# Kernel tuning notes

Measured on AMD Instinct MI355X. Metric: run time of the kernel, lower is better.

The kernel has to match this reference:

```python
import jax, jax.numpy as jnp
import numpy as np

N = 8192
MARGIN = 0.2
LAMB = 0.012
ITERS = 5


def setup_inputs() -> dict:
    key = jax.random.key(0)
    # sims in [0,1): cosine-similarity-like scores; exp(-(1-s)/lamb) needs s near [0,1]
    sims = jax.random.uniform(key, (N, N), dtype=jnp.float32)
    return {"sims": sims}


def _ot(sims):
    # Sinkhorn-Knopp normalization, r = c = ones so (r/u) == 1/u, (c/v) == 1/v
    P = jnp.exp(-(1.0 - sims) / LAMB)
    P = P / jnp.sum(P)  # global normalization (dims [-2,-1])
    for _ in range(ITERS):
        u = P.sum(axis=-1, keepdims=True)   # row sums  [N,1]
        P = P / u
        v = P.sum(axis=-2, keepdims=True)   # col sums  [1,N]
        P = P / v
    return P


def reference(sims):
    P = _ot(sims)
    d = jnp.diagonal(P)                     # [N]
    eye = jnp.eye(P.shape[0], dtype=bool)
    # cost_im: anchor = column diagonal (d[j]); cost_s: anchor = row diagonal (d[i])
    cost_im = jnp.where(eye, 0.0, jnp.maximum(P - d[None, :] + MARGIN, 0.0))
    cost_s = jnp.where(eye, 0.0, jnp.maximum(P - d[:, None] + MARGIN, 0.0))
    # max_violation = False -> sum over all hinge terms
    return cost_s.sum() + cost_im.sum()
```

## Files before the change

### kernel.cpp

```cpp
#include <hip/hip_runtime.h>


#define NN 8192u
#define MARGIN 0.2f
#define KF (1.4426950408889634f / 0.012f)

__device__ __forceinline__ float blk_reduce(float v, float* red) {
#pragma unroll
  for (int off = 32; off; off >>= 1) v += __shfl_down(v, off, 64);
  const int lane = threadIdx.x & 63, wid = threadIdx.x >> 6;
  __syncthreads();
  if (lane == 0) red[wid] = v;
  __syncthreads();
  return red[0] + red[1] + red[2] + red[3];
}

__device__ __forceinline__ void unpk4(uint q, float& f0, float& f1, float& f2,
                                      float& f3) {
  auto lo = __builtin_amdgcn_cvt_pk_f32_fp8((int)q, false);
  auto hi = __builtin_amdgcn_cvt_pk_f32_fp8((int)q, true);
  f0 = lo[0]; f1 = lo[1]; f2 = hi[0]; f3 = hi[1];
}

template <bool USEQ>
__global__ __launch_bounds__(256) void k_pass0(const float* __restrict__ sims,
                                               uint* __restrict__ Qw,
                                               float* __restrict__ R) {
  __shared__ float red[4];
  const uint row = blockIdx.x;
  const uint t = threadIdx.x;
  float acc = 0.f;
#pragma unroll
  for (uint ch = 0; ch < 8; ++ch) {
    const uint col = ch * 1024u + t * 4u;
    const float4 s = *(const float4*)(sims + row * NN + col);
    const float p0 = exp2f((s.x - 1.f) * KF);
    const float p1 = exp2f((s.y - 1.f) * KF);
    const float p2 = exp2f((s.z - 1.f) * KF);
    const float p3 = exp2f((s.w - 1.f) * KF);
    if constexpr (USEQ) {
      int pk = 0;
      pk = __builtin_amdgcn_cvt_pk_fp8_f32(p0, p1, pk, false);
      pk = __builtin_amdgcn_cvt_pk_fp8_f32(p2, p3, pk, true);
      Qw[(row * NN + col) >> 2] = (uint)pk;
      float q0, q1, q2, q3;
      unpk4((uint)pk, q0, q1, q2, q3);
      acc += (q0 + q1) + (q2 + q3);
    } else {
      acc += (p0 + p1) + (p2 + p3);
    }
  }
  const float s = blk_reduce(acc, red);
  if (t == 0) R[row] = 1.f / s;
}

template <bool USEQ>
__global__ __launch_bounds__(256) void k_colmv(const float* __restrict__ sims,
                                               const uint* __restrict__ Qw,
                                               const float* __restrict__ R,
                                               float* __restrict__ part) {
  const uint t = threadIdx.x;
  const uint col = blockIdx.x * 1024u + t * 4u;
  const uint row0 = blockIdx.y * 128u;
  float a0 = 0.f, a1 = 0.f, a2 = 0.f, a3 = 0.f;
  for (uint rr = 0; rr < 128u; ++rr) {
    const uint row = row0 + rr;
    const float Rr = R[row];
    if constexpr (USEQ) {
      float f0, f1, f2, f3;
      unpk4(Qw[(row * NN + col) >> 2], f0, f1, f2, f3);
      a0 += f0 * Rr; a1 += f1 * Rr; a2 += f2 * Rr; a3 += f3 * Rr;
    } else {
      const float4 s = *(const float4*)(sims + row * NN + col);
      a0 += exp2f((s.x - 1.f) * KF) * Rr;
      a1 += exp2f((s.y - 1.f) * KF) * Rr;
      a2 += exp2f((s.z - 1.f) * KF) * Rr;
      a3 += exp2f((s.w - 1.f) * KF) * Rr;
    }
  }
  float4 o; o.x = a0; o.y = a1; o.z = a2; o.w = a3;
  *(float4*)(part + blockIdx.y * NN + col) = o;
}

template <bool USEQ>
__global__ __launch_bounds__(256) void k_colred(const float* __restrict__ part,
                                                float* __restrict__ Cg, int fin,
                                                const float* __restrict__ sims,
                                                const uint* __restrict__ Qw,
                                                const float* __restrict__ R,
                                                float* __restrict__ dvec,
                                                float* __restrict__ out) {
  const uint j = blockIdx.x * 256u + threadIdx.x;
  float s = 0.f;
#pragma unroll 8
  for (uint r = 0; r < 64u; ++r) s += part[r * NN + j];
  const float c = 1.f / s;
  Cg[j] = c;
  if (fin) {
    float pd;
    if constexpr (USEQ) {
      const uint u = Qw[(j * 8193u) >> 2];
      const uint b = (u >> ((j & 3u) * 8u)) & 0xFFu;
      pd = __builtin_amdgcn_cvt_f32_fp8((int)b, 0);
    } else {
      pd = exp2f((sims[j * 8193u] - 1.f) * KF);
    }
    dvec[j] = pd * R[j] * c;
    if (j == 0) *out = 0.f;
  }
}

template <bool USEQ>
__global__ __launch_bounds__(256) void k_rowmv(const float* __restrict__ sims,
                                               const uint* __restrict__ Qw,
                                               const float* __restrict__ Cg,
                                               float* __restrict__ R) {
  __shared__ float ldsC[NN];
  __shared__ float red[4];
  const uint t = threadIdx.x;
  for (uint c = t * 4u; c < NN; c += 1024u)
    *(float4*)(ldsC + c) = *(const float4*)(Cg + c);
  __syncthreads();
#pragma unroll
  for (uint r = 0; r < 4u; ++r) {
    const uint row = blockIdx.x * 4u + r;
    float acc = 0.f;
#pragma unroll
    for (uint ch = 0; ch < 2u; ++ch) {
      const uint col = ch * 4096u + t * 16u;
      const float4 c0 = *(const float4*)(ldsC + col);
      const float4 c1 = *(const float4*)(ldsC + col + 4);
      const float4 c2 = *(const float4*)(ldsC + col + 8);
      const float4 c3 = *(const float4*)(ldsC + col + 12);
      if constexpr (USEQ) {
        const uint4 q = *(const uint4*)(Qw + row * 2048u + (col >> 2));
        float a0, a1, a2, a3, b0, b1, b2, b3;
        unpk4(q.x, a0, a1, a2, a3);
        unpk4(q.y, b0, b1, b2, b3);
        acc += a0 * c0.x + a1 * c0.y + a2 * c0.z + a3 * c0.w;
        acc += b0 * c1.x + b1 * c1.y + b2 * c1.z + b3 * c1.w;
        unpk4(q.z, a0, a1, a2, a3);
        unpk4(q.w, b0, b1, b2, b3);
        acc += a0 * c2.x + a1 * c2.y + a2 * c2.z + a3 * c2.w;
        acc += b0 * c3.x + b1 * c3.y + b2 * c3.z + b3 * c3.w;
      } else {
        const float* sp = sims + row * NN + col;
        const float4 s0 = *(const float4*)(sp);
        const float4 s1 = *(const float4*)(sp + 4);
        const float4 s2 = *(const float4*)(sp + 8);
        const float4 s3 = *(const float4*)(sp + 12);
        acc += exp2f((s0.x - 1.f) * KF) * c0.x + exp2f((s0.y - 1.f) * KF) * c0.y +
               exp2f((s0.z - 1.f) * KF) * c0.z + exp2f((s0.w - 1.f) * KF) * c0.w;
        acc += exp2f((s1.x - 1.f) * KF) * c1.x + exp2f((s1.y - 1.f) * KF) * c1.y +
               exp2f((s1.z - 1.f) * KF) * c1.z + exp2f((s1.w - 1.f) * KF) * c1.w;
        acc += exp2f((s2.x - 1.f) * KF) * c2.x + exp2f((s2.y - 1.f) * KF) * c2.y +
               exp2f((s2.z - 1.f) * KF) * c2.z + exp2f((s2.w - 1.f) * KF) * c2.w;
        acc += exp2f((s3.x - 1.f) * KF) * c3.x + exp2f((s3.y - 1.f) * KF) * c3.y +
               exp2f((s3.z - 1.f) * KF) * c3.z + exp2f((s3.w - 1.f) * KF) * c3.w;
      }
    }
    const float s = blk_reduce(acc, red);
    if (t == 0) R[row] = 1.f / s;
  }
}

template <bool USEQ>
__global__ __launch_bounds__(256) void k_loss(const float* __restrict__ sims,
                                              const uint* __restrict__ Qw,
                                              const float* __restrict__ R,
                                              const float* __restrict__ Cg,
                                              const float* __restrict__ dvec,
                                              float* __restrict__ out) {
  __shared__ float red[4];
  const uint t = threadIdx.x;
  const uint col = blockIdx.x * 1024u + t * 4u;
  const uint row0 = blockIdx.y * 128u;
  const float4 c4 = *(const float4*)(Cg + col);
  const float4 d4 = *(const float4*)(dvec + col);
  float acc = 0.f;
  for (uint rr = 0; rr < 128u; ++rr) {
    const uint row = row0 + rr;
    const float Rr = R[row];
    const float dr = dvec[row];
    float f0, f1, f2, f3;
    if constexpr (USEQ) {
      unpk4(Qw[(row * NN + col) >> 2], f0, f1, f2, f3);
    } else {
      const float4 s = *(const float4*)(sims + row * NN + col);
      f0 = exp2f((s.x - 1.f) * KF);
      f1 = exp2f((s.y - 1.f) * KF);
      f2 = exp2f((s.z - 1.f) * KF);
      f3 = exp2f((s.w - 1.f) * KF);
    }
    float p, h;
    p = f0 * Rr * c4.x;
    h = fmaxf(p - d4.x + MARGIN, 0.f) + fmaxf(p - dr + MARGIN, 0.f);
    acc += (row == col + 0u) ? 0.f : h;
    p = f1 * Rr * c4.y;
    h = fmaxf(p - d4.y + MARGIN, 0.f) + fmaxf(p - dr + MARGIN, 0.f);
    acc += (row == col + 1u) ? 0.f : h;
    p = f2 * Rr * c4.z;
    h = fmaxf(p - d4.z + MARGIN, 0.f) + fmaxf(p - dr + MARGIN, 0.f);
    acc += (row == col + 2u) ? 0.f : h;
    p = f3 * Rr * c4.w;
    h = fmaxf(p - d4.w + MARGIN, 0.f) + fmaxf(p - dr + MARGIN, 0.f);
    acc += (row == col + 3u) ? 0.f : h;
  }
  const float s = blk_reduce(acc, red);
  if (t == 0) atomicAdd(out, s);
}

template <bool USEQ>
static void run_all(const float* sims, float* out, void* ws, hipStream_t stream) {
  uint* Qw;
  float* R;
  if (USEQ) {
    Qw = (uint*)ws;
    R = (float*)((char*)ws + (size_t)NN * NN);
  } else {
    Qw = nullptr;
    R = (float*)ws;
  }
  float* C = R + NN;
  float* dv = C + NN;
  float* part = dv + NN;

  k_pass0<USEQ><<<8192, 256, 0, stream>>>(sims, Qw, R);
  for (int it = 0; it < 5; ++it) {
    k_colmv<USEQ><<<dim3(8, 64), 256, 0, stream>>>(sims, Qw, R, part);
    k_colred<USEQ><<<32, 256, 0, stream>>>(part, C, (it == 4) ? 1 : 0, sims, Qw,
                                           R, dv, out);
    if (it < 4) k_rowmv<USEQ><<<2048, 256, 0, stream>>>(sims, Qw, C, R);
  }
  k_loss<USEQ><<<dim3(8, 64), 256, 0, stream>>>(sims, Qw, R, C, dv, out);
}

extern "C" void kernel_launch(void* const* d_in, const int* in_sizes, int n_in,
                              void* d_out, int out_size, void* d_ws,
                              size_t ws_size, hipStream_t stream) {
  const float* sims = (const float*)d_in[0];
  float* out = (float*)d_out;
  const size_t need_q =
      (size_t)NN * NN + (size_t)(3 * NN + 64 * NN) * sizeof(float);
  if (ws_size >= need_q) {
    run_all<true>(sims, out, d_ws, stream);
  } else {
    run_all<false>(sims, out, d_ws, stream);
  }
}
```

Before: 538.5 us.

## Retune Sinkhorn kernels: more column-split blocks, vectorized row reduce, nontemporal loads

The column matvec now splits rows into 128 chunks of 64 instead of 64 chunks of 128, giving more blocks and more partial sums. The column-reduce kernel uses 1024 threads and combines the partials in shared memory. The row matvec drops the 8192-float LDS staging of column scales and instead processes four rows at once with coalesced per-row loads and a 4-way shuffle reduction. It also adds a nontemporal load for sims in pass0 and unroll pragmas, which could trade register pressure and workspace size for better occupancy and memory-level parallelism.

Result: faster. 485.7 us (-9.8%).

```diff
diff --git a/kernel.cpp b/kernel.cpp
--- a/kernel.cpp
+++ b/kernel.cpp
@@ -4,6 +4,8 @@
 #define NN 8192u
 #define MARGIN 0.2f
 #define KF (1.4426950408889634f / 0.012f)
+
+typedef float f32x4 __attribute__((ext_vector_type(4)));
 
 __device__ __forceinline__ float blk_reduce(float v, float* red) {
 #pragma unroll
@@ -33,11 +35,12 @@
 #pragma unroll
   for (uint ch = 0; ch < 8; ++ch) {
     const uint col = ch * 1024u + t * 4u;
-    const float4 s = *(const float4*)(sims + row * NN + col);
-    const float p0 = exp2f((s.x - 1.f) * KF);
-    const float p1 = exp2f((s.y - 1.f) * KF);
-    const float p2 = exp2f((s.z - 1.f) * KF);
-    const float p3 = exp2f((s.w - 1.f) * KF);
+    const f32x4 s =
+        __builtin_nontemporal_load((const f32x4*)(sims + row * NN + col));
+    const float p0 = exp2f((s[0] - 1.f) * KF);
+    const float p1 = exp2f((s[1] - 1.f) * KF);
+    const float p2 = exp2f((s[2] - 1.f) * KF);
+    const float p3 = exp2f((s[3] - 1.f) * KF);
     if constexpr (USEQ) {
       int pk = 0;
       pk = __builtin_amdgcn_cvt_pk_fp8_f32(p0, p1, pk, false);
@@ -61,9 +64,10 @@
                                                float* __restrict__ part) {
   const uint t = threadIdx.x;
   const uint col = blockIdx.x * 1024u + t * 4u;
-  const uint row0 = blockIdx.y * 128u;
+  const uint row0 = blockIdx.y * 64u;
   float a0 = 0.f, a1 = 0.f, a2 = 0.f, a3 = 0.f;
-  for (uint rr = 0; rr < 128u; ++rr) {
+#pragma unroll 8
+  for (uint rr = 0; rr < 64u; ++rr) {
     const uint row = row0 + rr;
     const float Rr = R[row];
     if constexpr (USEQ) {
@@ -83,30 +87,40 @@
 }
 
 template <bool USEQ>
-__global__ __launch_bounds__(256) void k_colred(const float* __restrict__ part,
-                                                float* __restrict__ Cg, int fin,
-                                                const float* __restrict__ sims,
-                                                const uint* __restrict__ Qw,
-                                                const float* __restrict__ R,
-                                                float* __restrict__ dvec,
-                                                float* __restrict__ out) {
-  const uint j = blockIdx.x * 256u + threadIdx.x;
+__global__ __launch_bounds__(1024) void k_colred(const float* __restrict__ part,
+                                                 float* __restrict__ Cg, int fin,
+                                                 const float* __restrict__ sims,
+                                                 const uint* __restrict__ Qw,
+                                                 const float* __restrict__ R,
+                                                 float* __restrict__ dvec,
+                                                 float* __restrict__ out) {
+  __shared__ float red2[3][256];
+  const uint t = threadIdx.x;
+  const uint lj = t & 255u;
+  const uint q = t >> 8;
+  const uint j = blockIdx.x * 256u + lj;
   float s = 0.f;
+  const uint r0 = q * 32u;
 #pragma unroll 8
-  for (uint r = 0; r < 64u; ++r) s += part[r * NN + j];
-  const float c = 1.f / s;
-  Cg[j] = c;
-  if (fin) {
-    float pd;
-    if constexpr (USEQ) {
-      const uint u = Qw[(j * 8193u) >> 2];
-      const uint b = (u >> ((j & 3u) * 8u)) & 0xFFu;
-      pd = __builtin_amdgcn_cvt_f32_fp8((int)b, 0);
-    } else {
-      pd = exp2f((sims[j * 8193u] - 1.f) * KF);
-    }
-    dvec[j] = pd * R[j] * c;
-    if (j == 0) *out = 0.f;
+  for (uint r = r0; r < r0 + 32u; ++r) s += part[r * NN + j];
+  if (q) red2[q - 1][lj] = s;
+  __syncthreads();
+  if (q == 0) {
+    s += red2[0][lj] + red2[1][lj] + red2[2][lj];
+    const float c = 1.f / s;
+    Cg[j] = c;
+    if (fin) {
+      float pd;
+      if constexpr (USEQ) {
+        const uint u = Qw[(j * 8193u) >> 2];
+        const uint b = (u >> ((j & 3u) * 8u)) & 0xFFu;
+        pd = __builtin_amdgcn_cvt_f32_fp8((int)b, 0);
+      } else {
+        pd = exp2f((sims[j * 8193u] - 1.f) * KF);
+      }
+      dvec[j] = pd * R[j] * c;
+      if (j == 0) *out = 0.f;
+    }
   }
 }
 
@@ -115,52 +129,55 @@
                                                const uint* __restrict__ Qw,
                                                const float* __restrict__ Cg,
                                                float* __restrict__ R) {
-  __shared__ float ldsC[NN];
-  __shared__ float red[4];
-  const uint t = threadIdx.x;
-  for (uint c = t * 4u; c < NN; c += 1024u)
-    *(float4*)(ldsC + c) = *(const float4*)(Cg + c);
-  __syncthreads();
-#pragma unroll
-  for (uint r = 0; r < 4u; ++r) {
-    const uint row = blockIdx.x * 4u + r;
-    float acc = 0.f;
-#pragma unroll
-    for (uint ch = 0; ch < 2u; ++ch) {
-      const uint col = ch * 4096u + t * 16u;
-      const float4 c0 = *(const float4*)(ldsC + col);
-      const float4 c1 = *(const float4*)(ldsC + col + 4);
-      const float4 c2 = *(const float4*)(ldsC + col + 8);
-      const float4 c3 = *(const float4*)(ldsC + col + 12);
-      if constexpr (USEQ) {
-        const uint4 q = *(const uint4*)(Qw + row * 2048u + (col >> 2));
-        float a0, a1, a2, a3, b0, b1, b2, b3;
-        unpk4(q.x, a0, a1, a2, a3);
-        unpk4(q.y, b0, b1, b2, b3);
-        acc += a0 * c0.x + a1 * c0.y + a2 * c0.z + a3 * c0.w;
-        acc += b0 * c1.x + b1 * c1.y + b2 * c1.z + b3 * c1.w;
-        unpk4(q.z, a0, a1, a2, a3);
-        unpk4(q.w, b0, b1, b2, b3);
-        acc += a0 * c2.x + a1 * c2.y + a2 * c2.z + a3 * c2.w;
-        acc += b0 * c3.x + b1 * c3.y + b2 * c3.z + b3 * c3.w;
-      } else {
-        const float* sp = sims + row * NN + col;
-        const float4 s0 = *(const float4*)(sp);
-        const float4 s1 = *(const float4*)(sp + 4);
-        const float4 s2 = *(const float4*)(sp + 8);
-        const float4 s3 = *(const float4*)(sp + 12);
-        acc += exp2f((s0.x - 1.f) * KF) * c0.x + exp2f((s0.y - 1.f) * KF) * c0.y +
-               exp2f((s0.z - 1.f) * KF) * c0.z + exp2f((s0.w - 1.f) * KF) * c0.w;
-        acc += exp2f((s1.x - 1.f) * KF) * c1.x + exp2f((s1.y - 1.f) * KF) * c1.y +
-               exp2f((s1.z - 1.f) * KF) * c1.z + exp2f((s1.w - 1.f) * KF) * c1.w;
-        acc += exp2f((s2.x - 1.f) * KF) * c2.x + exp2f((s2.y - 1.f) * KF) * c2.y +
-               exp2f((s2.z - 1.f) * KF) * c2.z + exp2f((s2.w - 1.f) * KF) * c2.w;
-        acc += exp2f((s3.x - 1.f) * KF) * c3.x + exp2f((s3.y - 1.f) * KF) * c3.y +
-               exp2f((s3.z - 1.f) * KF) * c3.z + exp2f((s3.w - 1.f) * KF) * c3.w;
-      }
-    }
-    const float s = blk_reduce(acc, red);
-    if (t == 0) R[row] = 1.f / s;
+  __shared__ float red[4][4];
+  const uint t = threadIdx.x;
+  const uint row0 = blockIdx.x * 4u;
+  float a0 = 0.f, a1 = 0.f, a2 = 0.f, a3 = 0.f;
+#pragma unroll
+  for (uint it = 0; it < 8u; ++it) {
+    const uint col = it * 1024u + t * 4u;
+    const float4 c = *(const float4*)(Cg + col);
+    if constexpr (USEQ) {
+      const uint base = (row0 * NN + col) >> 2;
+      float f0, f1, f2, f3;
+      unpk4(Qw[base         ], f0, f1, f2, f3);
+      a0 += f0 * c.x + f1 * c.y + f2 * c.z + f3 * c.w;
+      unpk4(Qw[base + 2048u ], f0, f1, f2, f3);
+      a1 += f0 * c.x + f1 * c.y + f2 * c.z + f3 * c.w;
+      unpk4(Qw[base + 4096u ], f0, f1, f2, f3);
+      a2 += f0 * c.x + f1 * c.y + f2 * c.z + f3 * c.w;
+      unpk4(Qw[base + 6144u ], f0, f1, f2, f3);
+      a3 += f0 * c.x + f1 * c.y + f2 * c.z + f3 * c.w;
+    } else {
+      const float* sp = sims + row0 * NN + col;
+      const float4 s0 = *(const float4*)(sp);
+      const float4 s1 = *(const float4*)(sp + NN);
+      const float4 s2 = *(const float4*)(sp + 2u * NN);
+      const float4 s3 = *(const float4*)(sp + 3u * NN);
+      a0 += exp2f((s0.x - 1.f) * KF) * c.x + exp2f((s0.y - 1.f) * KF) * c.y +
+            exp2f((s0.z - 1.f) * KF) * c.z + exp2f((s0.w - 1.f) * KF) * c.w;
+      a1 += exp2f((s1.x - 1.f) * KF) * c.x + exp2f((s1.y - 1.f) * KF) * c.y +
+            exp2f((s1.z - 1.f) * KF) * c.z + exp2f((s1.w - 1.f) * KF) * c.w;
+      a2 += exp2f((s2.x - 1.f) * KF) * c.x + exp2f((s2.y - 1.f) * KF) * c.y +
+            exp2f((s2.z - 1.f) * KF) * c.z + exp2f((s2.w - 1.f) * KF) * c.w;
+      a3 += exp2f((s3.x - 1.f) * KF) * c.x + exp2f((s3.y - 1.f) * KF) * c.y +
+            exp2f((s3.z - 1.f) * KF) * c.z + exp2f((s3.w - 1.f) * KF) * c.w;
+    }
+  }
+#pragma unroll
+  for (int off = 32; off; off >>= 1) {
+    a0 += __shfl_down(a0, off, 64);
+    a1 += __shfl_down(a1, off, 64);
+    a2 += __shfl_down(a2, off, 64);
+    a3 += __shfl_down(a3, off, 64);
+  }
+  const uint lane = t & 63u, wid = t >> 6;
+  if (lane == 0) {
+    red[wid][0] = a0; red[wid][1] = a1; red[wid][2] = a2; red[wid][3] = a3;
+  }
+  __syncthreads();
+  if (t < 4u) {
+    R[row0 + t] = 1.f / (red[0][t] + red[1][t] + red[2][t] + red[3][t]);
   }
 }
 
@@ -178,6 +195,7 @@
   const float4 c4 = *(const float4*)(Cg + col);
   const float4 d4 = *(const float4*)(dvec + col);
   float acc = 0.f;
+#pragma unroll 4
   for (uint rr = 0; rr < 128u; ++rr) {
     const uint row = row0 + rr;
     const float Rr = R[row];
@@ -227,9 +245,9 @@
 
   k_pass0<USEQ><<<8192, 256, 0, stream>>>(sims, Qw, R);
   for (int it = 0; it < 5; ++it) {
-    k_colmv<USEQ><<<dim3(8, 64), 256, 0, stream>>>(sims, Qw, R, part);
-    k_colred<USEQ><<<32, 256, 0, stream>>>(part, C, (it == 4) ? 1 : 0, sims, Qw,
-                                           R, dv, out);
+    k_colmv<USEQ><<<dim3(8, 128), 256, 0, stream>>>(sims, Qw, R, part);
+    k_colred<USEQ><<<32, 1024, 0, stream>>>(part, C, (it == 4) ? 1 : 0, sims,
+                                            Qw, R, dv, out);
     if (it < 4) k_rowmv<USEQ><<<2048, 256, 0, stream>>>(sims, Qw, C, R);
   }
   k_loss<USEQ><<<dim3(8, 64), 256, 0, stream>>>(sims, Qw, R, C, dv, out);
@@ -241,7 +259,7 @@
   const float* sims = (const float*)d_in[0];
   float* out = (float*)d_out;
   const size_t need_q =
-      (size_t)NN * NN + (size_t)(3 * NN + 64 * NN) * sizeof(float);
+      (size_t)NN * NN + (size_t)(3 * NN + 128 * NN) * sizeof(float);
   if (ws_size >= need_q) {
     run_all<true>(sims, out, d_ws, stream);
   } else {
```
